# Kernel optimization log

Hardware: AMD Instinct MI355X
Metric: run time of the kernel (lower is better)

## Reference

```python
import jax, jax.numpy as jnp
import numpy as np

K = 15  # kNN neighbors, matches init kwarg


def _knn_edges(x, k):
    # brute-force kNN, flow='target_to_source': row = center node, col = neighbor
    sq = jnp.sum(x * x, axis=-1)
    d2 = sq[:, None] - 2.0 * (x @ x.T) + sq[None, :]          # [N,N]
    n = x.shape[0]
    d2 = jnp.where(jnp.eye(n, dtype=bool), jnp.inf, d2)        # exclude self-loops
    _, idx = jax.lax.top_k(-d2, k)                             # [N,k] nearest
    row = jnp.repeat(jnp.arange(n), k)
    col = idx.reshape(-1)
    return jnp.stack([row, col])                               # [2, N*k]


def _scatter_softmax(a, seg, n):
    m = jax.ops.segment_max(a, seg, num_segments=n)
    m = jnp.where(jnp.isfinite(m), m, 0.0)
    e = jnp.exp(a - m[seg])
    s = jax.ops.segment_sum(e, seg, num_segments=n)
    return e / s[seg]


def _devconv(x, edges, W_theta, b_theta, W_phi, b_phi):
    # DevConv (neural mesh simplification): W_phi . max_{j in N(i)} W_theta(x_i - x_j)
    row, col = edges[0], edges[1]
    h = (x[row] - x[col]) @ W_theta.T + b_theta                # [E, H]
    agg = jax.ops.segment_max(h, row, num_segments=x.shape[0])  # [N, H]
    agg = jnp.where(jnp.isfinite(agg), agg, 0.0)               # guard empty rows
    return agg @ W_phi.T + b_phi


def setup_inputs() -> dict:
    key = jax.random.key(0)
    ks = jax.random.split(key, 8)
    N, E, H, C = 4096, 65536, 64, 3
    x = jax.random.normal(ks[0], (N, C), dtype=jnp.float32)
    edge_index = jax.random.randint(ks[1], (2, E), 0, N, dtype=jnp.int64)
    s_in, s_h = 1.0 / np.sqrt(C), 1.0 / np.sqrt(H)
    return {
        "x": x,
        "edge_index": edge_index,
        "W_theta": jax.random.normal(ks[2], (H, C), dtype=jnp.float32) * s_in,
        "b_theta": jnp.zeros((H,), dtype=jnp.float32),
        "W_phi": jax.random.normal(ks[3], (H, H), dtype=jnp.float32) * s_h,
        "b_phi": jnp.zeros((H,), dtype=jnp.float32),
        "W_q": jax.random.normal(ks[4], (H, H), dtype=jnp.float32) * s_h,
        "W_k": jax.random.normal(ks[5], (H, H), dtype=jnp.float32) * s_h,
    }


def reference(x, edge_index, W_theta, b_theta, W_phi, b_phi, W_q, W_k):
    n = x.shape[0]
    knn = _knn_edges(x, K)
    extended = jnp.concatenate([edge_index, knn], axis=1)
    feats = _devconv(x, extended, W_theta, b_theta, W_phi, b_phi)  # [N, H]
    row, col = edge_index[0], edge_index[1]
    q = feats @ W_q.T
    kf = feats @ W_k.T
    attn = jnp.sum(q[row] * kf[col], axis=-1)                  # [E]
    scores = _scatter_softmax(attn, row, n)                     # [E]
    # S, A as dense NxN (duplicates summed, matching sparse coalescing)
    S = jnp.zeros((n, n), dtype=x.dtype).at[row, col].add(scores)
    A = jnp.zeros((n, n), dtype=x.dtype).at[row, col].add(1.0)
    A_s = S @ A @ S.T                                           # simplified adjacency
    return A_s
```

## Files before the change

### kernel.cpp

```cpp
#include <hip/hip_runtime.h>
#include <math.h>

#define HN 64
#define KNN 15

__device__ __forceinline__ unsigned fenc(float f){
  unsigned u = __float_as_uint(f);
  return (u & 0x80000000u) ? ~u : (u | 0x80000000u);
}
__device__ __forceinline__ float fdec(unsigned u){
  return (u & 0x80000000u) ? __uint_as_float(u & 0x7fffffffu) : __uint_as_float(~u);
}

__device__ __forceinline__ unsigned long long u64min(unsigned long long a, unsigned long long b){
  return a < b ? a : b;
}
__device__ __forceinline__ unsigned long long shfl_xor_u64(unsigned long long v, int mask){
  unsigned lo = (unsigned)v, hi = (unsigned)(v >> 32);
  lo = __shfl_xor((int)lo, mask, 64);
  hi = __shfl_xor((int)hi, mask, 64);
  return ((unsigned long long)hi << 32) | lo;
}

__global__ void k_flag(const void* ei, int* flag, int n){
  __shared__ int ok[256];
  int t = threadIdx.x;
  long long v = ((const long long*)ei)[t];
  ok[t] = (v >= 0 && v < (long long)n) ? 1 : 0;
  __syncthreads();
  for (int off = 128; off > 0; off >>= 1){
    if (t < off) ok[t] &= ok[t + off];
    __syncthreads();
  }
  if (t == 0) *flag = ok[0];
}

__device__ __forceinline__ void edge_rc(const void* ei, int is64, int E, int e, int& r, int& c){
  if (is64){
    r = (int)((const long long*)ei)[e];
    c = (int)((const long long*)ei)[E + e];
  } else {
    r = ((const int*)ei)[e];
    c = ((const int*)ei)[E + e];
  }
}

__global__ void __launch_bounds__(256) k_knn(const float* __restrict__ x,
                                             int* __restrict__ knn_cols, int n){
  __shared__ unsigned denc[4096];
  __shared__ unsigned long long mk[256];
  int i = blockIdx.x, t = threadIdx.x;
  float xi0 = x[i*3], xi1 = x[i*3+1], xi2 = x[i*3+2];
  float sqi = xi0*xi0 + xi1*xi1 + xi2*xi2;
  unsigned long long best = ~0ULL;
  #pragma unroll
  for (int m = 0; m < 16; ++m){
    int j = t + 256*m;
    float a = x[j*3], b = x[j*3+1], c = x[j*3+2];
    float sqj = a*a + b*b + c*c;
    float dot = xi0*a + xi1*b + xi2*c;
    float d2 = (sqi - 2.0f*dot) + sqj;
    unsigned e = (j == i) ? 0xFFFFFFFFu : fenc(d2);
    denc[j] = e;
    unsigned long long key = ((unsigned long long)e << 32) | (unsigned)j;
    best = u64min(best, key);
  }
  mk[t] = best;
  __syncthreads();
  if (t >= 64) return;
  unsigned long long k0 = mk[t], k1 = mk[t+64], k2 = mk[t+128], k3 = mk[t+192];
  for (int m = 0; m < KNN; ++m){
    unsigned long long mm = u64min(u64min(k0, k1), u64min(k2, k3));
    #pragma unroll
    for (int off = 1; off < 64; off <<= 1)
      mm = u64min(mm, shfl_xor_u64(mm, off));
    int j = (int)(mm & 0xFFFFFFFFu);
    if (t == 0) knn_cols[i*KNN + m] = j;
    if ((j & 63) == t){
      int slot = j & 255;
      denc[j] = 0xFFFFFFFFu;
      unsigned long long nb = ~0ULL;
      #pragma unroll
      for (int m2 = 0; m2 < 16; ++m2){
        int jj = slot + 256*m2;
        unsigned long long key = ((unsigned long long)denc[jj] << 32) | (unsigned)jj;
        nb = u64min(nb, key);
      }
      int kreg = (j >> 6) & 3;
      if (kreg == 0) k0 = nb; else if (kreg == 1) k1 = nb;
      else if (kreg == 2) k2 = nb; else k3 = nb;
    }
  }
}

__global__ void k_y(const float* __restrict__ x, const float* __restrict__ Wt,
                    float* __restrict__ y, int n){
  int gid = blockIdx.x * 256 + threadIdx.x;
  if (gid >= n * HN) return;
  int nn = gid >> 6, h = gid & 63;
  float acc = x[nn*3] * Wt[h*3] + x[nn*3+1] * Wt[h*3+1] + x[nn*3+2] * Wt[h*3+2];
  y[gid] = acc;
}

__global__ void k_cnt(const void* ei, const int* flag, int* cnt, int* ccnt, int E){
  int e = blockIdx.x * 256 + threadIdx.x;
  if (e >= E) return;
  int r, c;
  edge_rc(ei, *flag, E, e, r, c);
  atomicAdd(&cnt[r], 1);
  atomicAdd(&ccnt[c], 1);
}

__global__ void k_scan(const int* __restrict__ cnt, int* __restrict__ ptr, int n){
  __shared__ int part[1024];
  int t = threadIdx.x;
  int base = t * 4;
  int a0 = cnt[base], a1 = cnt[base+1], a2 = cnt[base+2], a3 = cnt[base+3];
  int s = a0 + a1 + a2 + a3;
  part[t] = s;
  __syncthreads();
  for (int off = 1; off < 1024; off <<= 1){
    int v = (t >= off) ? part[t - off] : 0;
    __syncthreads();
    part[t] += v;
    __syncthreads();
  }
  int excl = part[t] - s;
  ptr[base]   = excl;
  ptr[base+1] = excl + a0;
  ptr[base+2] = excl + a0 + a1;
  ptr[base+3] = excl + a0 + a1 + a2;
  if (t == 1023) ptr[n] = part[1023];
}

__global__ void k_fillo(const void* ei, const int* flag, const int* __restrict__ ptr,
                        int* __restrict__ fillo, int* __restrict__ ecol, int E){
  int e = blockIdx.x * 256 + threadIdx.x;
  if (e >= E) return;
  int r, c;
  edge_rc(ei, *flag, E, e, r, c);
  int pos = ptr[r] + KNN*r + atomicAdd(&fillo[r], 1);
  ecol[pos] = c;
}

__global__ void k_fillk(const int* __restrict__ ptr, const int* __restrict__ cnt,
                        const int* __restrict__ knncols, int* __restrict__ ecol, int n){
  int gid = blockIdx.x * 256 + threadIdx.x;
  if (gid >= n * KNN) return;
  int i = gid / KNN, m = gid - i * KNN;
  ecol[ptr[i] + KNN*i + cnt[i] + m] = knncols[gid];
}

__global__ void k_devmin(const int* __restrict__ ptr, const int* __restrict__ ecol,
                         const float* __restrict__ y, const float* __restrict__ bt,
                         float* __restrict__ agg, int n){
  int t = threadIdx.x;
  int i = blockIdx.x * 4 + (t >> 6);
  int h = t & 63;
  int beg = ptr[i] + KNN*i;
  int end = ptr[i+1] + KNN*(i+1);
  float m = INFINITY;
  for (int idx = beg; idx < end; ++idx){
    int c = ecol[idx];
    m = fminf(m, y[c*HN + h]);
  }
  agg[i*HN + h] = y[i*HN + h] + bt[h] - m;
}

__global__ void k_fqk(const float* __restrict__ agg, const float* __restrict__ Wp,
                      const float* __restrict__ bp, const float* __restrict__ Wq,
                      const float* __restrict__ Wk, float* __restrict__ q,
                      float* __restrict__ kf, int n){
  __shared__ float sag[256];
  __shared__ float sft[256];
  int t = threadIdx.x;
  int nb = blockIdx.x * 4;
  sag[t] = agg[(size_t)nb*HN + t];
  __syncthreads();
  int nn = t >> 6, h = t & 63;
  float acc = bp[h];
  #pragma unroll 8
  for (int c = 0; c < HN; ++c) acc += sag[nn*HN + c] * Wp[h*HN + c];
  sft[t] = acc;
  __syncthreads();
  float aq = 0.f, ak = 0.f;
  #pragma unroll 8
  for (int c = 0; c < HN; ++c){
    float f = sft[nn*HN + c];
    aq += f * Wq[h*HN + c];
    ak += f * Wk[h*HN + c];
  }
  q[(size_t)nb*HN + t] = aq;
  kf[(size_t)nb*HN + t] = ak;
}

__global__ void k_attn(const void* ei, const int* flag, const float* __restrict__ q,
                       const float* __restrict__ kf, float* __restrict__ attn,
                       unsigned* __restrict__ rowmax, int E){
  int e = blockIdx.x * 256 + threadIdx.x;
  if (e >= E) return;
  int r, c;
  edge_rc(ei, *flag, E, e, r, c);
  const float4* qr = (const float4*)(q + r*HN);
  const float4* kc = (const float4*)(kf + c*HN);
  float acc = 0.f;
  #pragma unroll
  for (int m = 0; m < HN/4; ++m){
    float4 a = qr[m], b = kc[m];
    acc += a.x*b.x + a.y*b.y + a.z*b.z + a.w*b.w;
  }
  attn[e] = acc;
  atomicMax(&rowmax[r], fenc(acc));
}

__global__ void k_exp(const void* ei, const int* flag, const float* __restrict__ attn,
                      const unsigned* __restrict__ rowmax, float* __restrict__ scores,
                      float* __restrict__ rowsum, int E){
  int e = blockIdx.x * 256 + threadIdx.x;
  if (e >= E) return;
  int r, c;
  edge_rc(ei, *flag, E, e, r, c);
  float ex = expf(attn[e] - fdec(rowmax[r]));
  scores[e] = ex;
  atomicAdd(&rowsum[r], ex);
}

__global__ void k_csr2(const void* ei, const int* flag, const float* __restrict__ scores,
                       const float* __restrict__ rowsum, const int* __restrict__ ptr,
                       const int* __restrict__ cptr, int* __restrict__ fill2,
                       int* __restrict__ cfill, int* __restrict__ scol,
                       float* __restrict__ sval, int2* __restrict__ csp, int E){
  int e = blockIdx.x * 256 + threadIdx.x;
  if (e >= E) return;
  int r, c;
  edge_rc(ei, *flag, E, e, r, c);
  float v = scores[e] / rowsum[r];
  int p1 = ptr[r] + atomicAdd(&fill2[r], 1);
  scol[p1] = c;
  sval[p1] = v;
  int p2 = cptr[c] + atomicAdd(&cfill[c], 1);
  csp[p2] = make_int2(r, __float_as_int(v));
}

__global__ void __launch_bounds__(256) k_prod(
    const int* __restrict__ ptr, const int* __restrict__ scol,
    const float* __restrict__ sval, const int* __restrict__ cptr,
    const int2* __restrict__ csp, float* __restrict__ out, int n){
  __shared__ float orow[4096];
  __shared__ int   sk[64];
  __shared__ float sv[64];
  __shared__ int   slen[64];
  __shared__ int   spre[65];
  int i = blockIdx.x, t = threadIdx.x;
  for (int j = t; j < n; j += 256) orow[j] = 0.f;
  int beg = ptr[i], len = ptr[i+1] - beg;
  for (int pc = 0; pc < len; pc += 64){
    __syncthreads();
    int pn = min(64, len - pc);
    if (t < pn){
      int k = scol[beg + pc + t];
      sk[t] = k;
      sv[t] = sval[beg + pc + t];
      slen[t] = ptr[k+1] - ptr[k];
    }
    __syncthreads();
    if (t == 0){
      int s = 0;
      for (int p = 0; p < pn; ++p){ spre[p] = s; s += slen[p]; }
      spre[pn] = s;
    }
    __syncthreads();
    int Q = spre[pn];
    for (int idx = t; idx < Q; idx += 256){
      int lo = 0, hi = pn - 1;
      while (lo < hi){
        int mid = (lo + hi + 1) >> 1;
        if (spre[mid] <= idx) lo = mid; else hi = mid - 1;
      }
      int k = sk[lo];
      float v = sv[lo];
      int qq = ptr[k] + (idx - spre[lo]);
      int l = scol[qq];
      int rb = cptr[l], re = cptr[l+1];
      for (int r = rb; r < re; ++r){
        int2 e2 = csp[r];
        atomicAdd(&orow[e2.x], v * __int_as_float(e2.y));
      }
    }
  }
  __syncthreads();
  for (int j = t; j < n; j += 256) out[(size_t)i * n + j] = orow[j];
}

extern "C" void kernel_launch(void* const* d_in, const int* in_sizes, int n_in,
                              void* d_out, int out_size, void* d_ws, size_t ws_size,
                              hipStream_t stream) {
  const float* x   = (const float*)d_in[0];
  const void*  ei  = d_in[1];
  const float* Wt  = (const float*)d_in[2];
  const float* bt  = (const float*)d_in[3];
  const float* Wp  = (const float*)d_in[4];
  const float* bp  = (const float*)d_in[5];
  const float* Wq  = (const float*)d_in[6];
  const float* Wk  = (const float*)d_in[7];
  float* out = (float*)d_out;

  const int N = in_sizes[0] / 3;
  const int E = in_sizes[1] / 2;

  char* p = (char*)d_ws;
  auto alloc = [&](size_t bytes) -> void* {
    void* r = (void*)p;
    p += (bytes + 255) & ~(size_t)255;
    return r;
  };
  int*      ctr     = (int*)     alloc((size_t)7*N*4);
  int*      cnt     = ctr;
  int*      ccnt    = ctr + N;
  int*      fillo   = ctr + 2*N;
  int*      fill2   = ctr + 3*N;
  int*      cfill   = ctr + 4*N;
  unsigned* rowmax  = (unsigned*)(ctr + 5*N);
  float*    rowsum  = (float*)   (ctr + 6*N);

  float*    y       = (float*)   alloc((size_t)N*HN*4);
  float*    agg     = (float*)   alloc((size_t)N*HN*4);
  float*    q       = (float*)   alloc((size_t)N*HN*4);
  float*    kf      = (float*)   alloc((size_t)N*HN*4);
  float*    attn    = (float*)   alloc((size_t)E*4);
  float*    scores  = (float*)   alloc((size_t)E*4);
  int*      ptrb    = (int*)     alloc((size_t)(N+1)*4);
  int*      cptrb   = (int*)     alloc((size_t)(N+1)*4);
  int*      ecol    = (int*)     alloc((size_t)(E + N*KNN)*4);
  int*      scol    = (int*)     alloc((size_t)E*4);
  float*    sval    = (float*)   alloc((size_t)E*4);
  int2*     csp     = (int2*)    alloc((size_t)E*8);
  int*      knncols = (int*)     alloc((size_t)N*KNN*4);
  int*      flag    = (int*)     alloc(256);

  hipMemsetAsync(ctr, 0, (size_t)7*N*4, stream);

  k_flag<<<1, 256, 0, stream>>>(ei, flag, N);
  k_knn<<<N, 256, 0, stream>>>(x, knncols, N);
  k_y<<<(N*HN + 255)/256, 256, 0, stream>>>(x, Wt, y, N);

  k_cnt<<<(E + 255)/256, 256, 0, stream>>>(ei, flag, cnt, ccnt, E);
  k_scan<<<1, 1024, 0, stream>>>(cnt, ptrb, N);
  k_scan<<<1, 1024, 0, stream>>>(ccnt, cptrb, N);

  k_fillo<<<(E + 255)/256, 256, 0, stream>>>(ei, flag, ptrb, fillo, ecol, E);
  k_fillk<<<(N*KNN + 255)/256, 256, 0, stream>>>(ptrb, cnt, knncols, ecol, N);

  k_devmin<<<N/4, 256, 0, stream>>>(ptrb, ecol, y, bt, agg, N);
  k_fqk<<<N/4, 256, 0, stream>>>(agg, Wp, bp, Wq, Wk, q, kf, N);

  k_attn<<<(E + 255)/256, 256, 0, stream>>>(ei, flag, q, kf, attn, rowmax, E);
  k_exp<<<(E + 255)/256, 256, 0, stream>>>(ei, flag, attn, rowmax, scores, rowsum, E);
  k_csr2<<<(E + 255)/256, 256, 0, stream>>>(ei, flag, scores, rowsum, ptrb, cptrb,
                                            fill2, cfill, scol, sval, csp, E);

  k_prod<<<N, 256, 0, stream>>>(ptrb, scol, sval, cptrb, csp, out, N);
}
```

Before: 328.4 us.

## Fuse launches into fewer kernels and compute softmax per row in CSR

Merges the y projection, edge counting and kNN into one horizontally fused launch, merges the two scans and the two fill kernels, and fuses the devconv min with the feature/q/k matmuls. Attention and softmax now run once per row over the CSR edge list with wave reductions, which removes the global atomicMax/atomicAdd passes and the separate attn, scores and scol buffers. The SpGEMM product kernel is rewritten to spread work across waves and lanes without the serial prefix and binary search, and it uses vectorised zeroing and stores. The int64/int32 dtype check is now done per wave with a ballot instead of in a separate flag kernel.

```diff
diff --git a/kernel.cpp b/kernel.cpp
--- a/kernel.cpp
+++ b/kernel.cpp
@@ -7,9 +7,6 @@
 __device__ __forceinline__ unsigned fenc(float f){
   unsigned u = __float_as_uint(f);
   return (u & 0x80000000u) ? ~u : (u | 0x80000000u);
-}
-__device__ __forceinline__ float fdec(unsigned u){
-  return (u & 0x80000000u) ? __uint_as_float(u & 0x7fffffffu) : __uint_as_float(~u);
 }
 
 __device__ __forceinline__ unsigned long long u64min(unsigned long long a, unsigned long long b){
@@ -22,48 +19,62 @@
   return ((unsigned long long)hi << 32) | lo;
 }
 
-__global__ void k_flag(const void* ei, int* flag, int n){
-  __shared__ int ok[256];
-  int t = threadIdx.x;
-  long long v = ((const long long*)ei)[t];
-  ok[t] = (v >= 0 && v < (long long)n) ? 1 : 0;
-  __syncthreads();
-  for (int off = 128; off > 0; off >>= 1){
-    if (t < off) ok[t] &= ok[t + off];
-    __syncthreads();
-  }
-  if (t == 0) *flag = ok[0];
-}
-
-__device__ __forceinline__ void edge_rc(const void* ei, int is64, int E, int e, int& r, int& c){
-  if (is64){
-    r = (int)((const long long*)ei)[e];
-    c = (int)((const long long*)ei)[E + e];
+__device__ __forceinline__ void edge_load(const void* ei, int E, int n, int e, int& r, int& c){
+  const long long* L = (const long long*)ei;
+  long long vr = L[e];
+  bool ok = (vr >= 0 && vr < (long long)n);
+  unsigned long long bal = __ballot(ok);
+  unsigned long long act = __ballot(true);
+  if (bal == act){
+    r = (int)vr;
+    c = (int)L[E + e];
   } else {
-    r = ((const int*)ei)[e];
-    c = ((const int*)ei)[E + e];
-  }
-}
-
-__global__ void __launch_bounds__(256) k_knn(const float* __restrict__ x,
-                                             int* __restrict__ knn_cols, int n){
+    const int* I = (const int*)ei;
+    r = I[e];
+    c = I[E + e];
+  }
+}
+
+__global__ void __launch_bounds__(256) k_mega(
+    const float* __restrict__ x, const float* __restrict__ Wt, const void* ei,
+    float* __restrict__ y, int* __restrict__ knn_cols,
+    int* __restrict__ cnt, int* __restrict__ ccnt,
+    int N, int E, int nbY, int nbC){
   __shared__ unsigned denc[4096];
   __shared__ unsigned long long mk[256];
-  int i = blockIdx.x, t = threadIdx.x;
+  int b = blockIdx.x, t = threadIdx.x;
+  if (b < nbY){
+    int gid = b * 256 + t;
+    if (gid < N * HN){
+      int nn = gid >> 6, h = gid & 63;
+      y[gid] = x[nn*3] * Wt[h*3] + x[nn*3+1] * Wt[h*3+1] + x[nn*3+2] * Wt[h*3+2];
+    }
+    return;
+  }
+  if (b < nbY + nbC){
+    int e = (b - nbY) * 256 + t;
+    if (e < E){
+      int r, c;
+      edge_load(ei, E, N, e, r, c);
+      atomicAdd(&cnt[r], 1);
+      atomicAdd(&ccnt[c], 1);
+    }
+    return;
+  }
+  int i = b - nbY - nbC;
   float xi0 = x[i*3], xi1 = x[i*3+1], xi2 = x[i*3+2];
   float sqi = xi0*xi0 + xi1*xi1 + xi2*xi2;
   unsigned long long best = ~0ULL;
   #pragma unroll
   for (int m = 0; m < 16; ++m){
     int j = t + 256*m;
-    float a = x[j*3], b = x[j*3+1], c = x[j*3+2];
-    float sqj = a*a + b*b + c*c;
-    float dot = xi0*a + xi1*b + xi2*c;
+    float a = x[j*3], bb = x[j*3+1], c = x[j*3+2];
+    float sqj = a*a + bb*bb + c*c;
+    float dot = xi0*a + xi1*bb + xi2*c;
     float d2 = (sqi - 2.0f*dot) + sqj;
     unsigned e = (j == i) ? 0xFFFFFFFFu : fenc(d2);
     denc[j] = e;
-    unsigned long long key = ((unsigned long long)e << 32) | (unsigned)j;
-    best = u64min(best, key);
+    best = u64min(best, ((unsigned long long)e << 32) | (unsigned)j);
   }
   mk[t] = best;
   __syncthreads();
@@ -83,8 +94,7 @@
       #pragma unroll
       for (int m2 = 0; m2 < 16; ++m2){
         int jj = slot + 256*m2;
-        unsigned long long key = ((unsigned long long)denc[jj] << 32) | (unsigned)jj;
-        nb = u64min(nb, key);
+        nb = u64min(nb, ((unsigned long long)denc[jj] << 32) | (unsigned)jj);
       }
       int kreg = (j >> 6) & 3;
       if (kreg == 0) k0 = nb; else if (kreg == 1) k1 = nb;
@@ -93,29 +103,14 @@
   }
 }
 
-__global__ void k_y(const float* __restrict__ x, const float* __restrict__ Wt,
-                    float* __restrict__ y, int n){
-  int gid = blockIdx.x * 256 + threadIdx.x;
-  if (gid >= n * HN) return;
-  int nn = gid >> 6, h = gid & 63;
-  float acc = x[nn*3] * Wt[h*3] + x[nn*3+1] * Wt[h*3+1] + x[nn*3+2] * Wt[h*3+2];
-  y[gid] = acc;
-}
-
-__global__ void k_cnt(const void* ei, const int* flag, int* cnt, int* ccnt, int E){
-  int e = blockIdx.x * 256 + threadIdx.x;
-  if (e >= E) return;
-  int r, c;
-  edge_rc(ei, *flag, E, e, r, c);
-  atomicAdd(&cnt[r], 1);
-  atomicAdd(&ccnt[c], 1);
-}
-
-__global__ void k_scan(const int* __restrict__ cnt, int* __restrict__ ptr, int n){
+__global__ void k_scan2(const int* __restrict__ cnt, int* __restrict__ ptr,
+                        const int* __restrict__ ccnt, int* __restrict__ cptr, int n){
   __shared__ int part[1024];
+  const int* src = (blockIdx.x == 0) ? cnt : ccnt;
+  int* dst = (blockIdx.x == 0) ? ptr : cptr;
   int t = threadIdx.x;
   int base = t * 4;
-  int a0 = cnt[base], a1 = cnt[base+1], a2 = cnt[base+2], a3 = cnt[base+3];
+  int a0 = src[base], a1 = src[base+1], a2 = src[base+2], a3 = src[base+3];
   int s = a0 + a1 + a2 + a3;
   part[t] = s;
   __syncthreads();
@@ -126,58 +121,53 @@
     __syncthreads();
   }
   int excl = part[t] - s;
-  ptr[base]   = excl;
-  ptr[base+1] = excl + a0;
-  ptr[base+2] = excl + a0 + a1;
-  ptr[base+3] = excl + a0 + a1 + a2;
-  if (t == 1023) ptr[n] = part[1023];
-}
-
-__global__ void k_fillo(const void* ei, const int* flag, const int* __restrict__ ptr,
-                        int* __restrict__ fillo, int* __restrict__ ecol, int E){
-  int e = blockIdx.x * 256 + threadIdx.x;
-  if (e >= E) return;
-  int r, c;
-  edge_rc(ei, *flag, E, e, r, c);
-  int pos = ptr[r] + KNN*r + atomicAdd(&fillo[r], 1);
-  ecol[pos] = c;
-}
-
-__global__ void k_fillk(const int* __restrict__ ptr, const int* __restrict__ cnt,
-                        const int* __restrict__ knncols, int* __restrict__ ecol, int n){
-  int gid = blockIdx.x * 256 + threadIdx.x;
-  if (gid >= n * KNN) return;
-  int i = gid / KNN, m = gid - i * KNN;
-  ecol[ptr[i] + KNN*i + cnt[i] + m] = knncols[gid];
-}
-
-__global__ void k_devmin(const int* __restrict__ ptr, const int* __restrict__ ecol,
-                         const float* __restrict__ y, const float* __restrict__ bt,
-                         float* __restrict__ agg, int n){
+  dst[base]   = excl;
+  dst[base+1] = excl + a0;
+  dst[base+2] = excl + a0 + a1;
+  dst[base+3] = excl + a0 + a1 + a2;
+  if (t == 1023) dst[n] = part[1023];
+}
+
+__global__ void k_fill(const void* ei, const int* __restrict__ ptr,
+                       int* __restrict__ fillo, const int* __restrict__ cnt,
+                       const int* __restrict__ knncols, int* __restrict__ ecol,
+                       int N, int E, int nbE){
+  int b = blockIdx.x, t = threadIdx.x;
+  if (b < nbE){
+    int e = b * 256 + t;
+    if (e < E){
+      int r, c;
+      edge_load(ei, E, N, e, r, c);
+      int pos = ptr[r] + KNN*r + atomicAdd(&fillo[r], 1);
+      ecol[pos] = c;
+    }
+  } else {
+    int gid = (b - nbE) * 256 + t;
+    if (gid < N * KNN){
+      int i = gid / KNN, m = gid - i * KNN;
+      ecol[ptr[i] + KNN*i + cnt[i] + m] = knncols[gid];
+    }
+  }
+}
+
+__global__ void k_dev(const int* __restrict__ ptr, const int* __restrict__ ecol,
+                      const float* __restrict__ y, const float* __restrict__ bt,
+                      const float* __restrict__ Wp, const float* __restrict__ bp,
+                      const float* __restrict__ Wq, const float* __restrict__ Wk,
+                      float* __restrict__ q, float* __restrict__ kf, int n){
+  __shared__ float sag[256];
+  __shared__ float sft[256];
   int t = threadIdx.x;
   int i = blockIdx.x * 4 + (t >> 6);
   int h = t & 63;
   int beg = ptr[i] + KNN*i;
   int end = ptr[i+1] + KNN*(i+1);
   float m = INFINITY;
-  for (int idx = beg; idx < end; ++idx){
-    int c = ecol[idx];
-    m = fminf(m, y[c*HN + h]);
-  }
-  agg[i*HN + h] = y[i*HN + h] + bt[h] - m;
-}
-
-__global__ void k_fqk(const float* __restrict__ agg, const float* __restrict__ Wp,
-                      const float* __restrict__ bp, const float* __restrict__ Wq,
-                      const float* __restrict__ Wk, float* __restrict__ q,
-                      float* __restrict__ kf, int n){
-  __shared__ float sag[256];
-  __shared__ float sft[256];
-  int t = threadIdx.x;
-  int nb = blockIdx.x * 4;
-  sag[t] = agg[(size_t)nb*HN + t];
-  __syncthreads();
-  int nn = t >> 6, h = t & 63;
+  for (int idx = beg; idx < end; ++idx)
+    m = fminf(m, y[ecol[idx]*HN + h]);
+  sag[t] = y[i*HN + h] + bt[h] - m;
+  __syncthreads();
+  int nn = t >> 6;
   float acc = bp[h];
   #pragma unroll 8
   for (int c = 0; c < HN; ++c) acc += sag[nn*HN + c] * Wp[h*HN + c];
@@ -190,106 +180,89 @@
     aq += f * Wq[h*HN + c];
     ak += f * Wk[h*HN + c];
   }
-  q[(size_t)nb*HN + t] = aq;
-  kf[(size_t)nb*HN + t] = ak;
-}
-
-__global__ void k_attn(const void* ei, const int* flag, const float* __restrict__ q,
-                       const float* __restrict__ kf, float* __restrict__ attn,
-                       unsigned* __restrict__ rowmax, int E){
-  int e = blockIdx.x * 256 + threadIdx.x;
-  if (e >= E) return;
-  int r, c;
-  edge_rc(ei, *flag, E, e, r, c);
-  const float4* qr = (const float4*)(q + r*HN);
-  const float4* kc = (const float4*)(kf + c*HN);
-  float acc = 0.f;
+  size_t o = (size_t)blockIdx.x * 256 + t;
+  q[o] = aq;
+  kf[o] = ak;
+}
+
+__global__ void __launch_bounds__(256) k_rowattn(
+    const int* __restrict__ ptr, const int* __restrict__ cptr,
+    const int* __restrict__ ecol, const float* __restrict__ q,
+    const float* __restrict__ kf, float* __restrict__ sval,
+    int2* __restrict__ csp, int* __restrict__ cfill, int n){
+  int t = threadIdx.x;
+  int lane = t & 63;
+  int r = blockIdx.x * 4 + (t >> 6);
+  if (r >= n) return;
+  int base = ptr[r];
+  int deg = ptr[r+1] - base;
+  if (deg == 0) return;
+  int ebase = base + KNN*r;
+  float qh = q[(size_t)r*HN + lane];
+  float mx = -INFINITY;
+  for (int s = 0; s < deg; ++s){
+    int c = ecol[ebase + s];
+    float part = qh * kf[(size_t)c*HN + lane];
+    #pragma unroll
+    for (int off = 1; off < 64; off <<= 1) part += __shfl_xor(part, off, 64);
+    if (lane == 0) sval[base + s] = part;
+    mx = fmaxf(mx, part);
+  }
+  float lsum = 0.f;
+  for (int s = lane; s < deg; s += 64){
+    float e = expf(sval[base + s] - mx);
+    sval[base + s] = e;
+    lsum += e;
+  }
   #pragma unroll
-  for (int m = 0; m < HN/4; ++m){
-    float4 a = qr[m], b = kc[m];
-    acc += a.x*b.x + a.y*b.y + a.z*b.z + a.w*b.w;
-  }
-  attn[e] = acc;
-  atomicMax(&rowmax[r], fenc(acc));
-}
-
-__global__ void k_exp(const void* ei, const int* flag, const float* __restrict__ attn,
-                      const unsigned* __restrict__ rowmax, float* __restrict__ scores,
-                      float* __restrict__ rowsum, int E){
-  int e = blockIdx.x * 256 + threadIdx.x;
-  if (e >= E) return;
-  int r, c;
-  edge_rc(ei, *flag, E, e, r, c);
-  float ex = expf(attn[e] - fdec(rowmax[r]));
-  scores[e] = ex;
-  atomicAdd(&rowsum[r], ex);
-}
-
-__global__ void k_csr2(const void* ei, const int* flag, const float* __restrict__ scores,
-                       const float* __restrict__ rowsum, const int* __restrict__ ptr,
-                       const int* __restrict__ cptr, int* __restrict__ fill2,
-                       int* __restrict__ cfill, int* __restrict__ scol,
-                       float* __restrict__ sval, int2* __restrict__ csp, int E){
-  int e = blockIdx.x * 256 + threadIdx.x;
-  if (e >= E) return;
-  int r, c;
-  edge_rc(ei, *flag, E, e, r, c);
-  float v = scores[e] / rowsum[r];
-  int p1 = ptr[r] + atomicAdd(&fill2[r], 1);
-  scol[p1] = c;
-  sval[p1] = v;
-  int p2 = cptr[c] + atomicAdd(&cfill[c], 1);
-  csp[p2] = make_int2(r, __float_as_int(v));
+  for (int off = 1; off < 64; off <<= 1) lsum += __shfl_xor(lsum, off, 64);
+  for (int s = lane; s < deg; s += 64){
+    float v = sval[base + s] / lsum;
+    sval[base + s] = v;
+    int c = ecol[ebase + s];
+    int pos = cptr[c] + atomicAdd(&cfill[c], 1);
+    csp[pos] = make_int2(r, __float_as_int(v));
+  }
 }
 
 __global__ void __launch_bounds__(256) k_prod(
-    const int* __restrict__ ptr, const int* __restrict__ scol,
-    const float* __restrict__ sval, const int* __restrict__ cptr,
-    const int2* __restrict__ csp, float* __restrict__ out, int n){
+    const int* __restrict__ ptr, const int* __restrict__ cnt,
+    const int* __restrict__ ecol, const float* __restrict__ sval,
+    const int* __restrict__ cptr, const int2* __restrict__ csp,
+    float* __restrict__ out, int n){
   __shared__ float orow[4096];
-  __shared__ int   sk[64];
-  __shared__ float sv[64];
-  __shared__ int   slen[64];
-  __shared__ int   spre[65];
-  int i = blockIdx.x, t = threadIdx.x;
-  for (int j = t; j < n; j += 256) orow[j] = 0.f;
-  int beg = ptr[i], len = ptr[i+1] - beg;
-  for (int pc = 0; pc < len; pc += 64){
-    __syncthreads();
-    int pn = min(64, len - pc);
-    if (t < pn){
-      int k = scol[beg + pc + t];
-      sk[t] = k;
-      sv[t] = sval[beg + pc + t];
-      slen[t] = ptr[k+1] - ptr[k];
-    }
-    __syncthreads();
-    if (t == 0){
-      int s = 0;
-      for (int p = 0; p < pn; ++p){ spre[p] = s; s += slen[p]; }
-      spre[pn] = s;
-    }
-    __syncthreads();
-    int Q = spre[pn];
-    for (int idx = t; idx < Q; idx += 256){
-      int lo = 0, hi = pn - 1;
-      while (lo < hi){
-        int mid = (lo + hi + 1) >> 1;
-        if (spre[mid] <= idx) lo = mid; else hi = mid - 1;
-      }
-      int k = sk[lo];
-      float v = sv[lo];
-      int qq = ptr[k] + (idx - spre[lo]);
-      int l = scol[qq];
+  int t = threadIdx.x;
+  int lane = t & 63;
+  int w = t >> 6;
+  int i = blockIdx.x;
+  float4 z = {0.f, 0.f, 0.f, 0.f};
+  float4* o4 = (float4*)orow;
+  #pragma unroll
+  for (int ch = 0; ch < 4; ++ch) o4[ch*256 + t] = z;
+  __syncthreads();
+  int base = ptr[i];
+  int len = ptr[i+1] - base;
+  int ebase = base + KNN*i;
+  int qs = lane >> 2, rq = lane & 3;
+  for (int p = w; p < len; p += 4){
+    int k = ecol[ebase + p];
+    float v = sval[base + p];
+    int kbase = ptr[k];
+    int klen = ptr[k+1] - kbase;
+    int kebase = kbase + KNN*k;
+    for (int qq = qs; qq < klen; qq += 16){
+      int l = ecol[kebase + qq];
       int rb = cptr[l], re = cptr[l+1];
-      for (int r = rb; r < re; ++r){
-        int2 e2 = csp[r];
+      for (int rr = rb + rq; rr < re; rr += 4){
+        int2 e2 = csp[rr];
         atomicAdd(&orow[e2.x], v * __int_as_float(e2.y));
       }
     }
   }
   __syncthreads();
-  for (int j = t; j < n; j += 256) out[(size_t)i * n + j] = orow[j];
+  float4* dst = (float4*)(out + (size_t)i * n);
+  #pragma unroll
+  for (int ch = 0; ch < 4; ++ch) dst[ch*256 + t] = o4[ch*256 + t];
 }
 
 extern "C" void kernel_launch(void* const* d_in, const int* in_sizes, int n_in,
@@ -314,50 +287,34 @@
     p += (bytes + 255) & ~(size_t)255;
     return r;
   };
-  int*      ctr     = (int*)     alloc((size_t)7*N*4);
+  int*      ctr     = (int*)  alloc((size_t)4*N*4);
   int*      cnt     = ctr;
   int*      ccnt    = ctr + N;
-  int*      fillo   = ctr + 2*N;
-  int*      fill2   = ctr + 3*N;
-  int*      cfill   = ctr + 4*N;
-  unsigned* rowmax  = (unsigned*)(ctr + 5*N);
-  float*    rowsum  = (float*)   (ctr + 6*N);
-
-  float*    y       = (float*)   alloc((size_t)N*HN*4);
-  float*    agg     = (float*)   alloc((size_t)N*HN*4);
-  float*    q       = (float*)   alloc((size_t)N*HN*4);
-  float*    kf      = (float*)   alloc((size_t)N*HN*4);
-  float*    attn    = (float*)   alloc((size_t)E*4);
-  float*    scores  = (float*)   alloc((size_t)E*4);
-  int*      ptrb    = (int*)     alloc((size_t)(N+1)*4);
-  int*      cptrb   = (int*)     alloc((size_t)(N+1)*4);
-  int*      ecol    = (int*)     alloc((size_t)(E + N*KNN)*4);
-  int*      scol    = (int*)     alloc((size_t)E*4);
-  float*    sval    = (float*)   alloc((size_t)E*4);
-  int2*     csp     = (int2*)    alloc((size_t)E*8);
-  int*      knncols = (int*)     alloc((size_t)N*KNN*4);
-  int*      flag    = (int*)     alloc(256);
-
-  hipMemsetAsync(ctr, 0, (size_t)7*N*4, stream);
-
-  k_flag<<<1, 256, 0, stream>>>(ei, flag, N);
-  k_knn<<<N, 256, 0, stream>>>(x, knncols, N);
-  k_y<<<(N*HN + 255)/256, 256, 0, stream>>>(x, Wt, y, N);
-
-  k_cnt<<<(E + 255)/256, 256, 0, stream>>>(ei, flag, cnt, ccnt, E);
-  k_scan<<<1, 1024, 0, stream>>>(cnt, ptrb, N);
-  k_scan<<<1, 1024, 0, stream>>>(ccnt, cptrb, N);
-
-  k_fillo<<<(E + 255)/256, 256, 0, stream>>>(ei, flag, ptrb, fillo, ecol, E);
-  k_fillk<<<(N*KNN + 255)/256, 256, 0, stream>>>(ptrb, cnt, knncols, ecol, N);
-
-  k_devmin<<<N/4, 256, 0, stream>>>(ptrb, ecol, y, bt, agg, N);
-  k_fqk<<<N/4, 256, 0, stream>>>(agg, Wp, bp, Wq, Wk, q, kf, N);
-
-  k_attn<<<(E + 255)/256, 256, 0, stream>>>(ei, flag, q, kf, attn, rowmax, E);
-  k_exp<<<(E + 255)/256, 256, 0, stream>>>(ei, flag, attn, rowmax, scores, rowsum, E);
-  k_csr2<<<(E + 255)/256, 256, 0, stream>>>(ei, flag, scores, rowsum, ptrb, cptrb,
-                                            fill2, cfill, scol, sval, csp, E);
-
-  k_prod<<<N, 256, 0, stream>>>(ptrb, scol, sval, cptrb, csp, out, N);
-}
+  int*      cfill   = ctr + 2*N;
+  int*      fillo   = ctr + 3*N;
+
+  float*    y       = (float*)alloc((size_t)N*HN*4);
+  float*    q       = (float*)alloc((size_t)N*HN*4);
+  float*    kf      = (float*)alloc((size_t)N*HN*4);
+  int*      ptrb    = (int*)  alloc((size_t)(N+1)*4);
+  int*      cptrb   = (int*)  alloc((size_t)(N+1)*4);
+  int*      ecol    = (int*)  alloc((size_t)(E + N*KNN)*4);
+  float*    sval    = (float*)alloc((size_t)E*4);
+  int2*     csp     = (int2*) alloc((size_t)E*8);
+  int*      knncols = (int*)  alloc((size_t)N*KNN*4);
+
+  hipMemsetAsync(ctr, 0, (size_t)4*N*4, stream);
+
+  int nbY = (N*HN + 255)/256;
+  int nbC = (E + 255)/256;
+  int nbK = (N*KNN + 255)/256;
+
+  k_mega<<<nbY + nbC + N, 256, 0, stream>>>(x, Wt, ei, y, knncols, cnt, ccnt,
+                                            N, E, nbY, nbC);
+  k_scan2<<<2, 1024, 0, stream>>>(cnt, ptrb, ccnt, cptrb, N);
+  k_fill<<<nbC + nbK, 256, 0, stream>>>(ei, ptrb, fillo, cnt, knncols, ecol,
+                                        N, E, nbC);
+  k_dev<<<N/4, 256, 0, stream>>>(ptrb, ecol, y, bt, Wp, bp, Wq, Wk, q, kf, N);
+  k_rowattn<<<N/4, 256, 0, stream>>>(ptrb, cptrb, ecol, q, kf, sval, csp, cfill, N);
+  k_prod<<<N, 256, 0, stream>>>(ptrb, cnt, ecol, sval, cptrb, csp, out, N);
+}
```

Measured after the change: 297.3 us. 9.5% less time.
